# Performance work log

Hardware: AMD Instinct MI355X
Metric: run time of the kernel (lower is better)

The kernel has to match this reference:

```python
import jax, jax.numpy as jnp
import numpy as np

DN = ('NCDHW', 'OIDHW', 'NCDHW')
HEAD_COUNT = 8
LN_EPS = 1e-5


def _dwpw(x, dw_w, dw_b, pw_w, pw_b):
    # depthwise 3x3x3 conv (groups=C) followed by pointwise 1x1x1 conv, both with bias
    cin = x.shape[1]
    y = jax.lax.conv_general_dilated(x, dw_w, (1, 1, 1), [(1, 1), (1, 1), (1, 1)],
                                     dimension_numbers=DN, feature_group_count=cin)
    y = y + dw_b[None, :, None, None, None]
    y = jax.lax.conv_general_dilated(y, pw_w, (1, 1, 1), [(0, 0), (0, 0), (0, 0)],
                                     dimension_numbers=DN)
    return y + pw_b[None, :, None, None, None]


def setup_inputs() -> dict:
    key = jax.random.key(0)
    ks = iter(jax.random.split(key, 64))
    C, KC, VC = 256, 256, 256
    n, t, h, w = 4, 16, 28, 28
    d = {}
    d['input_rgb'] = jax.random.normal(next(ks), (n, C, t, h, w), dtype=jnp.float32)
    d['input_flow'] = jax.random.normal(next(ks), (n, C, t, h, w), dtype=jnp.float32)

    def conv_params(cin, cout, pfx):
        d[pfx + '_dw_w'] = jax.random.normal(next(ks), (cin, 1, 3, 3, 3), dtype=jnp.float32) * 0.05
        d[pfx + '_dw_b'] = jnp.zeros((cin,), dtype=jnp.float32)
        d[pfx + '_pw_w'] = jax.random.normal(next(ks), (cout, cin, 1, 1, 1), dtype=jnp.float32) * 0.05
        d[pfx + '_pw_b'] = jnp.zeros((cout,), dtype=jnp.float32)

    for s in ('rgb', 'flow'):
        for p, cout in (('k', KC), ('q', KC), ('v', VC)):
            conv_params(C, cout, f'{s}_{p}')
    conv_params(2 * VC, 2 * C, 'rp')
    return d


def reference(input_rgb, input_flow,
              rgb_k_dw_w, rgb_k_dw_b, rgb_k_pw_w, rgb_k_pw_b,
              rgb_q_dw_w, rgb_q_dw_b, rgb_q_pw_w, rgb_q_pw_b,
              rgb_v_dw_w, rgb_v_dw_b, rgb_v_pw_w, rgb_v_pw_b,
              flow_k_dw_w, flow_k_dw_b, flow_k_pw_w, flow_k_pw_b,
              flow_q_dw_w, flow_q_dw_b, flow_q_pw_w, flow_q_pw_b,
              flow_v_dw_w, flow_v_dw_b, flow_v_pw_w, flow_v_pw_b,
              rp_dw_w, rp_dw_b, rp_pw_w, rp_pw_b):
    n, C, t, h, w = input_rgb.shape
    S = t * h * w
    fused = jnp.concatenate([input_rgb, input_flow], axis=1)  # [n, 2C, t, h, w]

    def proj(x, dw_w, dw_b, pw_w, pw_b):
        return _dwpw(x, dw_w, dw_b, pw_w, pw_b).reshape(n, -1, S)

    keys = jnp.concatenate([proj(input_rgb, rgb_k_dw_w, rgb_k_dw_b, rgb_k_pw_w, rgb_k_pw_b),
                            proj(input_flow, flow_k_dw_w, flow_k_dw_b, flow_k_pw_w, flow_k_pw_b)], axis=1)
    queries = jnp.concatenate([proj(input_rgb, rgb_q_dw_w, rgb_q_dw_b, rgb_q_pw_w, rgb_q_pw_b),
                               proj(input_flow, flow_q_dw_w, flow_q_dw_b, flow_q_pw_w, flow_q_pw_b)], axis=1)
    values = jnp.concatenate([proj(input_rgb, rgb_v_dw_w, rgb_v_dw_b, rgb_v_pw_w, rgb_v_pw_b),
                              proj(input_flow, flow_v_dw_w, flow_v_dw_b, flow_v_pw_w, flow_v_pw_b)], axis=1)

    H = HEAD_COUNT
    hk = keys.shape[1] // H
    hv = values.shape[1] // H
    K = jax.nn.softmax(keys.reshape(n, H, hk, S), axis=3)      # softmax over sequence
    Q = jax.nn.softmax(queries.reshape(n, H, hk, S), axis=2)   # softmax over head channels
    V = values.reshape(n, H, hv, S)

    ctx = jnp.einsum('nhks,nhvs->nhkv', K, V)                   # [n,H,hk,hv]
    att = jnp.einsum('nhkv,nhks->nhvs', ctx, Q)                 # [n,H,hv,S]
    aggregated = att.reshape(n, H * hv, t, h, w)                # [n, 2*VC, t, h, w]

    rep = _dwpw(aggregated, rp_dw_w, rp_dw_b, rp_pw_w, rp_pw_b)
    x = rep + fused
    # f.layer_norm(x, x.size()): normalize over the ENTIRE tensor, no affine
    m = x.mean()
    v = x.var()
    return (x - m) / jnp.sqrt(v + LN_EPS)
```

## Files before the change

kernel.cpp:

```cpp
#include <hip/hip_runtime.h>
#include <math.h>


constexpr int NN = 4;
constexpr int C1 = 256;
constexpr int C2 = 512;
constexpr int TT = 16;
constexpr int SP = TT * 28 * 28;
constexpr long long NB = (long long)NN * C2 * SP;
constexpr int HEADS = 8;
constexpr int CTX_CHUNKS = 7;
constexpr int STATS_PARTS = 98 * 4 * 4;
constexpr double TOTAL_ELEMS = (double)NB;

typedef __attribute__((ext_vector_type(8))) short bf16x8;
typedef __attribute__((ext_vector_type(4))) short bf16x4;
typedef __attribute__((ext_vector_type(4))) float f32x4;

__device__ __forceinline__ short f2bf(float f)
{
    unsigned u = __float_as_uint(f);
    unsigned r = u + 0x7FFFu + ((u >> 16) & 1u);
    return (short)(r >> 16);
}
__device__ __forceinline__ float bf2f(short s)
{
    return __uint_as_float(((unsigned)(unsigned short)s) << 16);
}

__device__ __forceinline__ float4 loadvec4(const float* p)
{
    return *(const float4*)p;
}
__device__ __forceinline__ float4 loadvec4(const short* p)
{
    bf16x4 v = *(const bf16x4*)p;
    return (float4){bf2f(v[0]), bf2f(v[1]), bf2f(v[2]), bf2f(v[3])};
}

__device__ __forceinline__ void gload16(const short* g, short* l)
{
    __builtin_amdgcn_global_load_lds(
        (const __attribute__((address_space(1))) unsigned int*)g,
        (__attribute__((address_space(3))) unsigned int*)l,
        16, 0, 0);
}

__global__ __launch_bounds__(256)
void wcvt_kernel(const float* __restrict__ w0, const float* __restrict__ w1,
                 const float* __restrict__ w2, const float* __restrict__ w3,
                 const float* __restrict__ w4, const float* __restrict__ w5,
                 const float* __restrict__ w6, short* __restrict__ out)
{
    int i = blockIdx.x * 256 + threadIdx.x;
    if (i >= 655360) return;
    const float* src; int off;
    if (i < 393216) {
        int seg = i >> 16; off = i & 65535;
        src = seg == 0 ? w0 : seg == 1 ? w1 : seg == 2 ? w2
            : seg == 3 ? w3 : seg == 4 ? w4 : w5;
    } else { src = w6; off = i - 393216; }
    out[i] = f2bf(src[off]);
}

template<typename IT, int NSET>
__global__ __launch_bounds__(256)
void dwv_kernel(const IT* __restrict__ in,
                const float* __restrict__ w0c, const float* __restrict__ b0c,
                short* __restrict__ o0,
                const float* __restrict__ w1c, const float* __restrict__ b1c,
                short* __restrict__ o1,
                const float* __restrict__ w2c, const float* __restrict__ b2c,
                short* __restrict__ o2, int Cin)
{
    const int split = blockIdx.x, c = blockIdx.y, n = blockIdx.z;
    const int t0 = split * 8, t1 = t0 + 8;
    const int zs = (t0 - 1 > 0) ? t0 - 1 : 0;
    const int ze = (t1 < 15) ? t1 : 15;
    __shared__ float tile[2][900];
    const int tid = threadIdx.x;
    const size_t ibase = ((size_t)(n * Cin + c)) * TT * 784;
    const IT* inp = in + ibase;

    const float* wp[3] = {w0c, w1c, w2c};
    const float* bp[3] = {b0c, b1c, b2c};
    short* op[3] = {o0, o1, o2};
    float w[NSET][27], bv[NSET];
#pragma unroll
    for (int g = 0; g < NSET; ++g) {
#pragma unroll
        for (int i = 0; i < 27; ++i) w[g][i] = wp[g][c * 27 + i];
        bv[g] = bp[g][c];
    }

    for (int i = tid; i < 1800; i += 256) ((float*)tile)[i] = 0.f;

    const bool act = tid < 196;
    const int pos = tid * 4;
    const int hh = pos / 28, ww = pos - hh * 28;
    const int ladr = (hh + 1) * 30 + ww + 1;
    const int rbase = hh * 30 + ww;

    float4 preg = {0.f, 0.f, 0.f, 0.f};
    if (act) preg = loadvec4(inp + (size_t)zs * 784 + pos);

    float a0[NSET][4], a1[NSET][4], a2[NSET][4];
#pragma unroll
    for (int g = 0; g < NSET; ++g)
#pragma unroll
        for (int k = 0; k < 4; ++k) { a0[g][k] = bv[g]; a1[g][k] = bv[g]; a2[g][k] = bv[g]; }

    for (int z = zs; z <= ze; ++z) {
        float* tb = tile[z & 1];
        __syncthreads();
        if (act) {
            tb[ladr] = preg.x; tb[ladr + 1] = preg.y;
            tb[ladr + 2] = preg.z; tb[ladr + 3] = preg.w;
            if (z < ze) preg = loadvec4(inp + (size_t)(z + 1) * 784 + pos);
        }
        __syncthreads();
        if (act) {
            float v[3][6];
#pragma unroll
            for (int r = 0; r < 3; ++r)
#pragma unroll
                for (int j = 0; j < 6; ++j)
                    v[r][j] = tb[rbase + r * 30 + j];
#pragma unroll
            for (int g = 0; g < NSET; ++g)
#pragma unroll
                for (int dh = 0; dh < 3; ++dh)
#pragma unroll
                    for (int dw = 0; dw < 3; ++dw) {
                        const float wa = w[g][18 + dh * 3 + dw];
                        const float wb = w[g][9 + dh * 3 + dw];
                        const float wc2 = w[g][dh * 3 + dw];
#pragma unroll
                        for (int k = 0; k < 4; ++k) {
                            const float val = v[dh][k + dw];
                            a0[g][k] += val * wa;
                            a1[g][k] += val * wb;
                            a2[g][k] += val * wc2;
                        }
                    }
            if (z - 1 >= t0) {
#pragma unroll
                for (int g = 0; g < NSET; ++g) {
                    bf16x4 pk;
#pragma unroll
                    for (int k = 0; k < 4; ++k) pk[k] = f2bf(a0[g][k]);
                    *(bf16x4*)&op[g][ibase + (size_t)(z - 1) * 784 + pos] = pk;
                }
            }
#pragma unroll
            for (int g = 0; g < NSET; ++g)
#pragma unroll
                for (int k = 0; k < 4; ++k) {
                    a0[g][k] = a1[g][k]; a1[g][k] = a2[g][k]; a2[g][k] = bv[g];
                }
        }
    }
    if (act && ze >= t0 && ze < t1) {
#pragma unroll
        for (int g = 0; g < NSET; ++g) {
            bf16x4 pk;
#pragma unroll
            for (int k = 0; k < 4; ++k) pk[k] = f2bf(a0[g][k]);
            *(bf16x4*)&op[g][ibase + (size_t)ze * 784 + pos] = pk;
        }
    }
}

template<int MODE>
__global__ __launch_bounds__(256)
void pw_mfma_kernel(const short* __restrict__ Wb, const float* __restrict__ bias,
                    const short* __restrict__ act, short* __restrict__ outB,
                    float* __restrict__ outF, const float* __restrict__ rgb,
                    const float* __restrict__ flow, double* __restrict__ partials,
                    int Cin, size_t nStride, size_t cStride, int chOff)
{
    __shared__ short smem[34816];
    const int tid = threadIdx.x;
    const int w = tid >> 6, lane = tid & 63;
    const int s0 = blockIdx.x * 128;
    const int m0 = blockIdx.y * 128;
    const int n = blockIdx.z;
    const short* aSrc = Wb + (size_t)m0 * Cin;
    const short* bSrc = act + (size_t)n * Cin * SP;
    f32x4 acc[4][4];
#pragma unroll
    for (int i = 0; i < 4; ++i)
#pragma unroll
        for (int j = 0; j < 4; ++j)
            acc[i][j] = (f32x4){0.f, 0.f, 0.f, 0.f};
    const int lrow = lane >> 3, lslot = lane & 7;
    const int wr = w >> 1, wc = w & 1;
    const int kg = tid >> 4, scb = tid & 15;
    const int nt = Cin >> 6;

    {
        short* nA = smem;
        short* nB = smem + 16384;
#pragma unroll
        for (int cc = 0; cc < 4; ++cc) {
            const int chunk = w * 4 + cc;
            const int row = chunk * 8 + lrow;
            const int ss = lslot ^ (row & 7);
            gload16(aSrc + (size_t)row * Cin + ss * 8, &nA[chunk * 512]);
        }
        bf16x8 breg[4];
#pragma unroll
        for (int r = 0; r < 4; ++r)
            breg[r] = *(const bf16x8*)(bSrc + (size_t)(kg * 4 + r) * SP + s0 + scb * 8);
#pragma unroll
        for (int j = 0; j < 8; ++j) {
            bf16x4 pk;
#pragma unroll
            for (int r = 0; r < 4; ++r) pk[r] = breg[r][j];
            const int srow = scb * 8 + j;
            const int slot = (kg >> 1) ^ (scb & 7);
            *(bf16x4*)&nB[srow * 72 + slot * 8 + (kg & 1) * 4] = pk;
        }
    }
    __syncthreads();

    for (int t = 0; t < nt; ++t) {
        short* cA = smem + (t & 1) * 8192;
        short* cB = smem + 16384 + (t & 1) * 9216;
        short* nA = smem + ((t + 1) & 1) * 8192;
        short* nB = smem + 16384 + ((t + 1) & 1) * 9216;
        const bool more = (t + 1) < nt;
        bf16x8 bnext[4];
        if (more) {
            const int kt = (t + 1) << 6;
#pragma unroll
            for (int cc = 0; cc < 4; ++cc) {
                const int chunk = w * 4 + cc;
                const int row = chunk * 8 + lrow;
                const int ss = lslot ^ (row & 7);
                gload16(aSrc + (size_t)row * Cin + kt + ss * 8, &nA[chunk * 512]);
            }
#pragma unroll
            for (int r = 0; r < 4; ++r)
                bnext[r] = *(const bf16x8*)(bSrc + (size_t)(kt + kg * 4 + r) * SP + s0 + scb * 8);
        }
#pragma unroll
        for (int kf = 0; kf < 2; ++kf) {
            bf16x8 af[4], bfr[4];
            const int kb = kf * 4 + (lane >> 4);
#pragma unroll
            for (int i = 0; i < 4; ++i) {
                const int row = wr * 64 + i * 16 + (lane & 15);
                af[i] = *(const bf16x8*)&cA[row * 64 + ((kb ^ (row & 7)) << 3)];
            }
#pragma unroll
            for (int j = 0; j < 4; ++j) {
                const int srow = wc * 64 + j * 16 + (lane & 15);
                bfr[j] = *(const bf16x8*)&cB[srow * 72 + ((kb ^ ((srow >> 3) & 7)) << 3)];
            }
#pragma unroll
            for (int i = 0; i < 4; ++i)
#pragma unroll
                for (int j = 0; j < 4; ++j)
                    acc[i][j] = __builtin_amdgcn_mfma_f32_16x16x32_bf16(
                        af[i], bfr[j], acc[i][j], 0, 0, 0);
        }
        if (more) {
#pragma unroll
            for (int j = 0; j < 8; ++j) {
                bf16x4 pk;
#pragma unroll
                for (int r = 0; r < 4; ++r) pk[r] = bnext[r][j];
                const int srow = scb * 8 + j;
                const int slot = (kg >> 1) ^ (scb & 7);
                *(bf16x4*)&nB[srow * 72 + slot * 8 + (kg & 1) * 4] = pk;
            }
        }
        __syncthreads();
    }

    if constexpr (MODE == 0) {
        short* ep = smem;
#pragma unroll
        for (int i = 0; i < 4; ++i) {
            const int mloc = wr * 64 + i * 16 + (lane >> 4) * 4;
#pragma unroll
            for (int j = 0; j < 4; ++j) {
                const int sloc = wc * 64 + j * 16 + (lane & 15);
#pragma unroll
                for (int r = 0; r < 4; ++r)
                    ep[(mloc + r) * 136 + sloc] =
                        f2bf(acc[i][j][r] + bias[m0 + mloc + r]);
            }
        }
        __syncthreads();
        short* op = outB + (size_t)n * nStride;
#pragma unroll
        for (int cc = 0; cc < 8; ++cc) {
            const int idx = tid + cc * 256;
            const int mloc = idx >> 4, ch = idx & 15;
            bf16x8 v = *(const bf16x8*)&ep[mloc * 136 + ch * 8];
            *(bf16x8*)&op[(size_t)(chOff + m0 + mloc) * cStride + s0 + ch * 8] = v;
        }
    } else if constexpr (MODE == 1) {
        short* ep = smem;
#pragma unroll
        for (int i = 0; i < 4; ++i) {
            const int mb = wr * 64 + i * 16 + (lane >> 4) * 4;
#pragma unroll
            for (int j = 0; j < 4; ++j) {
                const int sloc = wc * 64 + j * 16 + (lane & 15);
                bf16x4 pk;
#pragma unroll
                for (int r = 0; r < 4; ++r)
                    pk[r] = f2bf(acc[i][j][r] + bias[m0 + mb + r]);
                *(bf16x4*)&ep[sloc * 136 + mb] = pk;
            }
        }
        __syncthreads();
#pragma unroll
        for (int cc = 0; cc < 8; ++cc) {
            const int idx = tid + cc * 256;
            const int sloc = idx >> 4, ch = idx & 15;
            bf16x8 v = *(const bf16x8*)&ep[sloc * 136 + ch * 8];
            *(bf16x8*)&outB[((size_t)n * SP + s0 + sloc) * 512 + chOff + m0 + ch * 8] = v;
        }
    } else {
        float* ep = (float*)smem;
        float* xp = outF + (size_t)n * C2 * SP;
        const float* rbase = (m0 < 256)
            ? rgb + ((size_t)n * 256 + m0) * SP
            : flow + ((size_t)n * 256 + (m0 - 256)) * SP;
        double ls = 0.0, lss = 0.0;
#pragma unroll
        for (int p = 0; p < 2; ++p) {
            if (p) __syncthreads();
            if (wr == p) {
#pragma unroll
                for (int i = 0; i < 4; ++i) {
                    const int mloc = i * 16 + (lane >> 4) * 4;
#pragma unroll
                    for (int j = 0; j < 4; ++j) {
                        const int sloc = wc * 64 + j * 16 + (lane & 15);
#pragma unroll
                        for (int r = 0; r < 4; ++r)
                            ep[(mloc + r) * 132 + sloc] =
                                acc[i][j][r] + bias[m0 + p * 64 + mloc + r];
                    }
                }
            }
            __syncthreads();
#pragma unroll
            for (int cc = 0; cc < 8; ++cc) {
                const int idx = tid + cc * 256;
                const int row = idx >> 5, ch = idx & 31;
                const int m = m0 + p * 64 + row;
                float4 a = *(const float4*)&ep[row * 132 + ch * 4];
                float4 rs = *(const float4*)&rbase[(size_t)(p * 64 + row) * SP + s0 + ch * 4];
                float4 x;
                x.x = a.x + rs.x; x.y = a.y + rs.y;
                x.z = a.z + rs.z; x.w = a.w + rs.w;
                *(float4*)&xp[(size_t)m * SP + s0 + ch * 4] = x;
                ls += (double)x.x + (double)x.y + (double)x.z + (double)x.w;
                lss += (double)x.x * x.x + (double)x.y * x.y +
                       (double)x.z * x.z + (double)x.w * x.w;
            }
        }
        __shared__ double s1[256], s2[256];
        s1[tid] = ls; s2[tid] = lss;
        __syncthreads();
        for (int st = 128; st > 0; st >>= 1) {
            if (tid < st) { s1[tid] += s1[tid + st]; s2[tid] += s2[tid + st]; }
            __syncthreads();
        }
        if (tid == 0) {
            const size_t bid = ((size_t)blockIdx.z * gridDim.y + blockIdx.y) *
                               gridDim.x + blockIdx.x;
            partials[2 * bid] = s1[0];
            partials[2 * bid + 1] = s2[0];
        }
    }
}

__global__ __launch_bounds__(256)
void row_stats_kernel(const short* __restrict__ K, float2* __restrict__ st)
{
    const short* p = K + (size_t)blockIdx.x * SP;
    __shared__ float sm[4];
    __shared__ float bc;
    const int tid = threadIdx.x, wv = tid >> 6, ln = tid & 63;
    float m = -1e30f;
    for (int c = tid; c < SP / 8; c += 256) {
        bf16x8 v = *(const bf16x8*)(p + c * 8);
#pragma unroll
        for (int j = 0; j < 8; ++j) m = fmaxf(m, bf2f(v[j]));
    }
    for (int o = 32; o; o >>= 1) m = fmaxf(m, __shfl_down(m, o, 64));
    if (ln == 0) sm[wv] = m;
    __syncthreads();
    if (tid == 0) bc = fmaxf(fmaxf(sm[0], sm[1]), fmaxf(sm[2], sm[3]));
    __syncthreads();
    m = bc;
    float sum = 0.f;
    for (int c = tid; c < SP / 8; c += 256) {
        bf16x8 v = *(const bf16x8*)(p + c * 8);
#pragma unroll
        for (int j = 0; j < 8; ++j) sum += __expf(bf2f(v[j]) - m);
    }
    for (int o = 32; o; o >>= 1) sum += __shfl_down(sum, o, 64);
    __syncthreads();
    if (ln == 0) sm[wv] = sum;
    __syncthreads();
    if (tid == 0) {
        float tot = sm[0] + sm[1] + sm[2] + sm[3];
        st[blockIdx.x] = (float2){m, 1.f / tot};
    }
}

__global__ __launch_bounds__(256)
void ctx_mfma_kernel(const short* __restrict__ Kb, const short* __restrict__ Vb,
                     const float2* __restrict__ stats, float* __restrict__ part)
{
    const int chunk = blockIdx.x, nh = blockIdx.y;
    const short* Kp = Kb + (size_t)nh * 64 * SP;
    const short* Vp = Vb + (size_t)nh * 64 * SP;
    __shared__ short lK[64 * 256];
    __shared__ short lV[64 * 256];
    const int tid = threadIdx.x;
    const int w = tid >> 6, lane = tid & 63;
    const int wr = w >> 1, wc = w & 1;
    f32x4 acc[2][2];
#pragma unroll
    for (int i = 0; i < 2; ++i)
#pragma unroll
        for (int j = 0; j < 2; ++j)
            acc[i][j] = (f32x4){0.f, 0.f, 0.f, 0.f};

    float km8[8], ki8[8];
#pragma unroll
    for (int ps = 0; ps < 8; ++ps) {
        float2 s = stats[nh * 64 + (tid >> 5) + ps * 8];
        km8[ps] = s.x; ki8[ps] = s.y;
    }

    for (int sub = 0; sub < 7; ++sub) {
        const int sOff = chunk * 1792 + sub * 256;
#pragma unroll
        for (int cc = 0; cc < 8; ++cc) {
            const int ch = w * 8 + cc;
            const int row = ch * 2 + (lane >> 5);
            const int sc = lane & 31;
            gload16(Vp + (size_t)row * SP + sOff + ((sc ^ (row & 7)) << 3),
                    &lV[ch * 512]);
        }
#pragma unroll
        for (int ps = 0; ps < 8; ++ps) {
            const int row = (tid >> 5) + ps * 8;
            const int sc = tid & 31;
            bf16x8 kv = *(const bf16x8*)(Kp + (size_t)row * SP + sOff + sc * 8);
            bf16x8 ev;
#pragma unroll
            for (int j = 0; j < 8; ++j)
                ev[j] = f2bf(__expf(bf2f(kv[j]) - km8[ps]) * ki8[ps]);
            *(bf16x8*)&lK[row * 256 + ((sc ^ (row & 7)) << 3)] = ev;
        }
        __syncthreads();
#pragma unroll
        for (int ks = 0; ks < 8; ++ks) {
            const int kb = ks * 4 + (lane >> 4);
            bf16x8 ak[2], bv[2];
#pragma unroll
            for (int i = 0; i < 2; ++i) {
                const int rk = wr * 32 + i * 16 + (lane & 15);
                ak[i] = *(const bf16x8*)&lK[rk * 256 + ((kb ^ (rk & 7)) << 3)];
            }
#pragma unroll
            for (int j = 0; j < 2; ++j) {
                const int rv = wc * 32 + j * 16 + (lane & 15);
                bv[j] = *(const bf16x8*)&lV[rv * 256 + ((kb ^ (rv & 7)) << 3)];
            }
#pragma unroll
            for (int i = 0; i < 2; ++i)
#pragma unroll
                for (int j = 0; j < 2; ++j)
                    acc[i][j] = __builtin_amdgcn_mfma_f32_16x16x32_bf16(
                        ak[i], bv[j], acc[i][j], 0, 0, 0);
        }
        __syncthreads();
    }
    float* op = part + ((size_t)nh * CTX_CHUNKS + chunk) * 4096;
#pragma unroll
    for (int i = 0; i < 2; ++i)
#pragma unroll
        for (int j = 0; j < 2; ++j)
#pragma unroll
            for (int r = 0; r < 4; ++r) {
                const int k = wr * 32 + i * 16 + (lane >> 4) * 4 + r;
                const int v = wc * 32 + j * 16 + (lane & 15);
                op[k * 64 + v] = acc[i][j][r];
            }
}

__global__ __launch_bounds__(256)
void ctx_reduce_kernel(const float* __restrict__ part, float* __restrict__ ctx)
{
    const int nh = blockIdx.x;
    for (int e = threadIdx.x; e < 4096; e += 256) {
        float s = 0.f;
        for (int c = 0; c < CTX_CHUNKS; ++c)
            s += part[((size_t)nh * CTX_CHUNKS + c) * 4096 + e];
        ctx[(size_t)nh * 4096 + e] = s;
    }
}

__global__ __launch_bounds__(256)
void att_kernel(const float* __restrict__ ctx, const short* __restrict__ Qb,
                short* __restrict__ out)
{
    const int nh = blockIdx.y;
    const int n = nh >> 3, h = nh & 7;
    const int s0 = blockIdx.x * 64;
    const float* cp = ctx + (size_t)nh * 4096;
    __shared__ short lC[64 * 64];
    __shared__ short lQ[64 * 64];
    __shared__ float red[64][4];
    __shared__ short lO[64 * 72];
    const int tid = threadIdx.x;
    const int w = tid >> 6, lane = tid & 63;

#pragma unroll
    for (int u = 0; u < 2; ++u) {
        const int si = (tid >> 6) + u * 4;
        const int v = tid & 63;
        bf16x8 pk;
#pragma unroll
        for (int j = 0; j < 8; ++j) pk[j] = f2bf(cp[(si * 8 + j) * 64 + v]);
        *(bf16x8*)&lC[v * 64 + ((si ^ (v & 7)) << 3)] = pk;
    }
    const int sq = tid >> 2, qpart = tid & 3;
    const short* Qrow = Qb + ((size_t)n * SP + s0 + sq) * 512 + h * 64 + qpart * 16;
    bf16x8 q0 = *(const bf16x8*)(Qrow);
    bf16x8 q1 = *(const bf16x8*)(Qrow + 8);
    float e[16];
    float mx = -1e30f;
#pragma unroll
    for (int j = 0; j < 8; ++j) {
        e[j] = bf2f(q0[j]); e[8 + j] = bf2f(q1[j]);
        mx = fmaxf(mx, fmaxf(e[j], e[8 + j]));
    }
    red[sq][qpart] = mx;
    __syncthreads();
    mx = fmaxf(fmaxf(red[sq][0], red[sq][1]), fmaxf(red[sq][2], red[sq][3]));
    float sum = 0.f;
#pragma unroll
    for (int j = 0; j < 16; ++j) { e[j] = __expf(e[j] - mx); sum += e[j]; }
    __syncthreads();
    red[sq][qpart] = sum;
    __syncthreads();
    const float sinv = 1.f / (red[sq][0] + red[sq][1] + red[sq][2] + red[sq][3]);
    bf16x8 p0, p1;
#pragma unroll
    for (int j = 0; j < 8; ++j) {
        p0[j] = f2bf(e[j] * sinv);
        p1[j] = f2bf(e[8 + j] * sinv);
    }
    *(bf16x8*)&lQ[sq * 64 + (((qpart * 2) ^ (sq & 7)) << 3)] = p0;
    *(bf16x8*)&lQ[sq * 64 + (((qpart * 2 + 1) ^ (sq & 7)) << 3)] = p1;
    __syncthreads();

    f32x4 acc[4];
#pragma unroll
    for (int i = 0; i < 4; ++i) acc[i] = (f32x4){0.f, 0.f, 0.f, 0.f};
    const int srow = w * 16 + (lane & 15);
#pragma unroll
    for (int ks = 0; ks < 2; ++ks) {
        const int kb = ks * 4 + (lane >> 4);
        bf16x8 bq = *(const bf16x8*)&lQ[srow * 64 + ((kb ^ (srow & 7)) << 3)];
#pragma unroll
        for (int i = 0; i < 4; ++i) {
            const int vr = i * 16 + (lane & 15);
            bf16x8 av = *(const bf16x8*)&lC[vr * 64 + ((kb ^ (vr & 7)) << 3)];
            acc[i] = __builtin_amdgcn_mfma_f32_16x16x32_bf16(av, bq, acc[i], 0, 0, 0);
        }
    }
#pragma unroll
    for (int i = 0; i < 4; ++i)
#pragma unroll
        for (int r = 0; r < 4; ++r)
            lO[(i * 16 + (lane >> 4) * 4 + r) * 72 + w * 16 + (lane & 15)] =
                f2bf(acc[i][r]);
    __syncthreads();
    short* op = out + (size_t)nh * 64 * SP;
#pragma unroll
    for (int cc = 0; cc < 2; ++cc) {
        const int idx = tid + cc * 256;
        const int v = idx >> 3, ch = idx & 7;
        bf16x8 t = *(const bf16x8*)&lO[v * 72 + ch * 8];
        *(bf16x8*)&op[(size_t)v * SP + s0 + ch * 8] = t;
    }
}

__global__ __launch_bounds__(256)
void stats_final_kernel(const double* __restrict__ partials, float* __restrict__ mv)
{
    double ls = 0.0, lss = 0.0;
    for (int i = threadIdx.x; i < STATS_PARTS; i += 256) {
        ls += partials[2 * i];
        lss += partials[2 * i + 1];
    }
    __shared__ double s1[256], s2[256];
    const int tid = threadIdx.x;
    s1[tid] = ls; s2[tid] = lss;
    __syncthreads();
    for (int s = 128; s > 0; s >>= 1) {
        if (tid < s) { s1[tid] += s1[tid + s]; s2[tid] += s2[tid + s]; }
        __syncthreads();
    }
    if (tid == 0) {
        double mean = s1[0] / TOTAL_ELEMS;
        double var = s2[0] / TOTAL_ELEMS - mean * mean;
        mv[0] = (float)mean;
        mv[1] = (float)(1.0 / sqrt(var + 1e-5));
    }
}

__global__ __launch_bounds__(256)
void normalize_kernel(float* __restrict__ x, const float* __restrict__ mv)
{
    const float mean = mv[0], inv = mv[1];
    size_t i = ((size_t)blockIdx.x * 256 + threadIdx.x) * 4;
    const size_t tot = (size_t)NB;
    const size_t step = (size_t)gridDim.x * 1024;
    for (; i < tot; i += step) {
        float4 v = *(float4*)&x[i];
        v.x = (v.x - mean) * inv; v.y = (v.y - mean) * inv;
        v.z = (v.z - mean) * inv; v.w = (v.w - mean) * inv;
        *(float4*)&x[i] = v;
    }
}

extern "C" void kernel_launch(void* const* d_in, const int* in_sizes, int n_in,
                              void* d_out, int out_size, void* d_ws, size_t ws_size,
                              hipStream_t stream)
{
    (void)in_sizes; (void)n_in; (void)out_size; (void)ws_size;
    const float* rgb = (const float*)d_in[0];
    const float* flow = (const float*)d_in[1];
    float* ws = (float*)d_ws;

    short* bufK = (short*)ws;
    short* bufQ = (short*)(ws + NB / 2);
    short* bufV = (short*)(ws + NB);
    short* actK = (short*)(ws + 3 * NB / 2);
    short* actQ = (short*)(ws + 7 * NB / 4);
    short* actV = (short*)(ws + 2 * NB);
    short* wB   = (short*)(ws + 9 * NB / 4);
    float2* rowStats = (float2*)(wB + 655360);
    float* ctxBuf = (float*)(rowStats + 2048);
    double* partials = (double*)(ctxBuf + 32 * 4096);
    float* mv = (float*)(partials + 2 * STATS_PARTS);
    float* ctxPart = ws + 3 * NB / 2;
    short* rpDw = actK;

    const size_t nsA = (size_t)C2 * SP, csA = SP;

    wcvt_kernel<<<2560, 256, 0, stream>>>(
        (const float*)d_in[4], (const float*)d_in[12], (const float*)d_in[16],
        (const float*)d_in[24], (const float*)d_in[8], (const float*)d_in[20],
        (const float*)d_in[28], wB);

    for (int st = 0; st < 2; ++st) {
        const float* src = st ? flow : rgb;
        const int kI = st ? 14 : 2, qI = st ? 18 : 6, vI = st ? 22 : 10;
        const int choff = st ? 256 : 0;
        dwv_kernel<float, 3><<<dim3(2, C1, NN), 256, 0, stream>>>(
            src,
            (const float*)d_in[kI], (const float*)d_in[kI + 1], actK,
            (const float*)d_in[qI], (const float*)d_in[qI + 1], actQ,
            (const float*)d_in[vI], (const float*)d_in[vI + 1], actV, C1);
        pw_mfma_kernel<0><<<dim3(SP / 128, 2, NN), 256, 0, stream>>>(
            wB + (size_t)(st ? 2 : 0) * 65536, (const float*)d_in[kI + 3], actK,
            bufK, nullptr, nullptr, nullptr, nullptr, C1, nsA, csA, choff);
        pw_mfma_kernel<0><<<dim3(SP / 128, 2, NN), 256, 0, stream>>>(
            wB + (size_t)(st ? 3 : 1) * 65536, (const float*)d_in[vI + 3], actV,
            bufV, nullptr, nullptr, nullptr, nullptr, C1, nsA, csA, choff);
        pw_mfma_kernel<1><<<dim3(SP / 128, 2, NN), 256, 0, stream>>>(
            wB + (size_t)(st ? 5 : 4) * 65536, (const float*)d_in[qI + 3], actQ,
            bufQ, nullptr, nullptr, nullptr, nullptr, C1, 0, 0, choff);
    }

    row_stats_kernel<<<NN * C2, 256, 0, stream>>>(bufK, rowStats);
    ctx_mfma_kernel<<<dim3(CTX_CHUNKS, NN * HEADS), 256, 0, stream>>>(
        bufK, bufV, rowStats, ctxPart);
    ctx_reduce_kernel<<<NN * HEADS, 256, 0, stream>>>(ctxPart, ctxBuf);
    att_kernel<<<dim3(SP / 64, NN * HEADS), 256, 0, stream>>>(
        ctxBuf, bufQ, bufV);

    dwv_kernel<short, 1><<<dim3(2, C2, NN), 256, 0, stream>>>(
        bufV, (const float*)d_in[26], (const float*)d_in[27], rpDw,
        nullptr, nullptr, nullptr, nullptr, nullptr, nullptr, C2);
    pw_mfma_kernel<2><<<dim3(SP / 128, 4, NN), 256, 0, stream>>>(
        wB + 6 * 65536, (const float*)d_in[29], rpDw, nullptr,
        (float*)d_out, rgb, flow, partials, C2, 0, 0, 0);

    stats_final_kernel<<<1, 256, 0, stream>>>(partials, mv);
    normalize_kernel<<<2048, 256, 0, stream>>>((float*)d_out, mv);
}
```

Measured before the change: 443.7 us.

## Fuse K softmax stats into K/V pointwise GEMM, bf16 intermediate before normalize

Merges the K and V pointwise GEMMs into a single launch and computes per-block online-softmax partial max/sum for K in the epilogue. A small reduce kernel then replaces the full re-read of K done by row_stats_kernel. The final pointwise epilogue now writes the residual sum as bf16 to a workspace buffer instead of fp32 to the output, and uses a remapped 1D grid to improve locality. The normalize pass reads bf16 and writes fp32, cutting memory traffic, at the cost of rounding the pre-normalization values to bf16.

Result: faster. 419.3 us (median of 2 runs) (-5.5%).

```diff
diff --git a/kernel.cpp b/kernel.cpp
--- a/kernel.cpp
+++ b/kernel.cpp
@@ -10,7 +10,8 @@
 constexpr long long NB = (long long)NN * C2 * SP;
 constexpr int HEADS = 8;
 constexpr int CTX_CHUNKS = 7;
-constexpr int STATS_PARTS = 98 * 4 * 4;
+constexpr int SBLKS = 98;
+constexpr int STATS_PARTS = SBLKS * 4 * 4;
 constexpr double TOTAL_ELEMS = (double)NB;
 
 typedef __attribute__((ext_vector_type(8))) short bf16x8;
@@ -173,20 +174,37 @@
 
 template<int MODE>
 __global__ __launch_bounds__(256)
-void pw_mfma_kernel(const short* __restrict__ Wb, const float* __restrict__ bias,
-                    const short* __restrict__ act, short* __restrict__ outB,
-                    float* __restrict__ outF, const float* __restrict__ rgb,
-                    const float* __restrict__ flow, double* __restrict__ partials,
+void pw_mfma_kernel(const short* __restrict__ WbA, const float* __restrict__ biasA,
+                    const short* __restrict__ actA, short* __restrict__ outA,
+                    const short* __restrict__ WbV, const float* __restrict__ biasV,
+                    const short* __restrict__ actV, short* __restrict__ outV,
+                    const float* __restrict__ rgb, const float* __restrict__ flow,
+                    double* __restrict__ partials, float2* __restrict__ kpart,
                     int Cin, size_t nStride, size_t cStride, int chOff)
 {
     __shared__ short smem[34816];
     const int tid = threadIdx.x;
     const int w = tid >> 6, lane = tid & 63;
-    const int s0 = blockIdx.x * 128;
-    const int m0 = blockIdx.y * 128;
-    const int n = blockIdx.z;
+    int s0, m0, n, seg = 0, sBlk;
+    if constexpr (MODE == 2) {
+        const int b = blockIdx.x;
+        const int r = b & 7, t = b >> 3;
+        const int mBlk = t & 3, q = t >> 2;
+        const int g = q * 8 + r;
+        n = g / SBLKS; sBlk = g % SBLKS;
+        s0 = sBlk * 128; m0 = mBlk * 128;
+    } else {
+        sBlk = blockIdx.x; s0 = sBlk * 128; n = blockIdx.z;
+        if constexpr (MODE == 0) { seg = blockIdx.y >> 1; m0 = (blockIdx.y & 1) * 128; }
+        else m0 = blockIdx.y * 128;
+    }
+    const short* Wb = (MODE == 0 && seg) ? WbV : WbA;
+    const float* bias = (MODE == 0 && seg) ? biasV : biasA;
+    const short* actp = (MODE == 0 && seg) ? actV : actA;
+    short* outB = (MODE == 0 && seg) ? outV : outA;
+
     const short* aSrc = Wb + (size_t)m0 * Cin;
-    const short* bSrc = act + (size_t)n * Cin * SP;
+    const short* bSrc = actp + (size_t)n * Cin * SP;
     f32x4 acc[4][4];
 #pragma unroll
     for (int i = 0; i < 4; ++i)
@@ -302,6 +320,23 @@
             bf16x8 v = *(const bf16x8*)&ep[mloc * 136 + ch * 8];
             *(bf16x8*)&op[(size_t)(chOff + m0 + mloc) * cStride + s0 + ch * 8] = v;
         }
+        if (seg == 0) {
+            const int row = tid >> 1, half = tid & 1;
+            const short* rp = &ep[row * 136 + half * 64];
+            float mx = -1e30f;
+#pragma unroll 8
+            for (int j = 0; j < 64; ++j) mx = fmaxf(mx, bf2f(rp[j]));
+            float sum = 0.f;
+#pragma unroll 8
+            for (int j = 0; j < 64; ++j) sum += __expf(bf2f(rp[j]) - mx);
+            const float mo = __shfl_xor(mx, 1, 64);
+            const float so = __shfl_xor(sum, 1, 64);
+            const float mg = fmaxf(mx, mo);
+            const float sg = sum * __expf(mx - mg) + so * __expf(mo - mg);
+            if (half == 0)
+                kpart[(size_t)(n * 512 + chOff + m0 + row) * SBLKS + sBlk] =
+                    (float2){mg, sg};
+        }
     } else if constexpr (MODE == 1) {
         short* ep = smem;
 #pragma unroll
@@ -323,47 +358,46 @@
             const int idx = tid + cc * 256;
             const int sloc = idx >> 4, ch = idx & 15;
             bf16x8 v = *(const bf16x8*)&ep[sloc * 136 + ch * 8];
-            *(bf16x8*)&outB[((size_t)n * SP + s0 + sloc) * 512 + chOff + m0 + ch * 8] = v;
+            *(bf16x8*)&outA[((size_t)n * SP + s0 + sloc) * 512 + chOff + m0 + ch * 8] = v;
         }
     } else {
         float* ep = (float*)smem;
-        float* xp = outF + (size_t)n * C2 * SP;
+#pragma unroll
+        for (int i = 0; i < 4; ++i) {
+            const int mloc = wr * 64 + i * 16 + (lane >> 4) * 4;
+#pragma unroll
+            for (int j = 0; j < 4; ++j) {
+                const int sloc = wc * 64 + j * 16 + (lane & 15);
+#pragma unroll
+                for (int r = 0; r < 4; ++r)
+                    ep[(mloc + r) * 132 + sloc] =
+                        acc[i][j][r] + bias[m0 + mloc + r];
+            }
+        }
+        __syncthreads();
+        short* xo = outA + (size_t)n * C2 * SP;
         const float* rbase = (m0 < 256)
             ? rgb + ((size_t)n * 256 + m0) * SP
             : flow + ((size_t)n * 256 + (m0 - 256)) * SP;
         double ls = 0.0, lss = 0.0;
 #pragma unroll
-        for (int p = 0; p < 2; ++p) {
-            if (p) __syncthreads();
-            if (wr == p) {
-#pragma unroll
-                for (int i = 0; i < 4; ++i) {
-                    const int mloc = i * 16 + (lane >> 4) * 4;
-#pragma unroll
-                    for (int j = 0; j < 4; ++j) {
-                        const int sloc = wc * 64 + j * 16 + (lane & 15);
-#pragma unroll
-                        for (int r = 0; r < 4; ++r)
-                            ep[(mloc + r) * 132 + sloc] =
-                                acc[i][j][r] + bias[m0 + p * 64 + mloc + r];
-                    }
-                }
-            }
-            __syncthreads();
-#pragma unroll
-            for (int cc = 0; cc < 8; ++cc) {
-                const int idx = tid + cc * 256;
-                const int row = idx >> 5, ch = idx & 31;
-                const int m = m0 + p * 64 + row;
-                float4 a = *(const float4*)&ep[row * 132 + ch * 4];
-                float4 rs = *(const float4*)&rbase[(size_t)(p * 64 + row) * SP + s0 + ch * 4];
-                float4 x;
-                x.x = a.x + rs.x; x.y = a.y + rs.y;
-                x.z = a.z + rs.z; x.w = a.w + rs.w;
-                *(float4*)&xp[(size_t)m * SP + s0 + ch * 4] = x;
-                ls += (double)x.x + (double)x.y + (double)x.z + (double)x.w;
-                lss += (double)x.x * x.x + (double)x.y * x.y +
-                       (double)x.z * x.z + (double)x.w * x.w;
+        for (int cc = 0; cc < 8; ++cc) {
+            const int idx = tid + cc * 256;
+            const int mloc = idx >> 4, ch = idx & 15;
+            float4 a0 = *(const float4*)&ep[mloc * 132 + ch * 8];
+            float4 a1 = *(const float4*)&ep[mloc * 132 + ch * 8 + 4];
+            float4 r0 = *(const float4*)&rbase[(size_t)mloc * SP + s0 + ch * 8];
+            float4 r1 = *(const float4*)&rbase[(size_t)mloc * SP + s0 + ch * 8 + 4];
+            bf16x8 pk;
+            pk[0] = f2bf(a0.x + r0.x); pk[1] = f2bf(a0.y + r0.y);
+            pk[2] = f2bf(a0.z + r0.z); pk[3] = f2bf(a0.w + r0.w);
+            pk[4] = f2bf(a1.x + r1.x); pk[5] = f2bf(a1.y + r1.y);
+            pk[6] = f2bf(a1.z + r1.z); pk[7] = f2bf(a1.w + r1.w);
+            *(bf16x8*)&xo[(size_t)(m0 + mloc) * SP + s0 + ch * 8] = pk;
+#pragma unroll
+            for (int k = 0; k < 8; ++k) {
+                const double xv = (double)bf2f(pk[k]);
+                ls += xv; lss += xv * xv;
             }
         }
         __shared__ double s1[256], s2[256];
@@ -374,47 +408,25 @@
             __syncthreads();
         }
         if (tid == 0) {
-            const size_t bid = ((size_t)blockIdx.z * gridDim.y + blockIdx.y) *
-                               gridDim.x + blockIdx.x;
-            partials[2 * bid] = s1[0];
-            partials[2 * bid + 1] = s2[0];
-        }
-    }
-}
-
-__global__ __launch_bounds__(256)
-void row_stats_kernel(const short* __restrict__ K, float2* __restrict__ st)
-{
-    const short* p = K + (size_t)blockIdx.x * SP;
-    __shared__ float sm[4];
-    __shared__ float bc;
-    const int tid = threadIdx.x, wv = tid >> 6, ln = tid & 63;
-    float m = -1e30f;
-    for (int c = tid; c < SP / 8; c += 256) {
-        bf16x8 v = *(const bf16x8*)(p + c * 8);
-#pragma unroll
-        for (int j = 0; j < 8; ++j) m = fmaxf(m, bf2f(v[j]));
-    }
-    for (int o = 32; o; o >>= 1) m = fmaxf(m, __shfl_down(m, o, 64));
-    if (ln == 0) sm[wv] = m;
-    __syncthreads();
-    if (tid == 0) bc = fmaxf(fmaxf(sm[0], sm[1]), fmaxf(sm[2], sm[3]));
-    __syncthreads();
-    m = bc;
-    float sum = 0.f;
-    for (int c = tid; c < SP / 8; c += 256) {
-        bf16x8 v = *(const bf16x8*)(p + c * 8);
-#pragma unroll
-        for (int j = 0; j < 8; ++j) sum += __expf(bf2f(v[j]) - m);
-    }
-    for (int o = 32; o; o >>= 1) sum += __shfl_down(sum, o, 64);
-    __syncthreads();
-    if (ln == 0) sm[wv] = sum;
-    __syncthreads();
-    if (tid == 0) {
-        float tot = sm[0] + sm[1] + sm[2] + sm[3];
-        st[blockIdx.x] = (float2){m, 1.f / tot};
-    }
+            partials[2 * blockIdx.x] = s1[0];
+            partials[2 * blockIdx.x + 1] = s2[0];
+        }
+    }
+}
+
+__global__ __launch_bounds__(256)
+void kstats_reduce_kernel(const float2* __restrict__ kpart, float2* __restrict__ st)
+{
+    const int row = blockIdx.x * 256 + threadIdx.x;
+    const float2* p = kpart + (size_t)row * SBLKS;
+    float m = -1e30f, s = 0.f;
+    for (int b = 0; b < SBLKS; ++b) {
+        float2 e = p[b];
+        float nm = fmaxf(m, e.x);
+        s = s * __expf(m - nm) + e.y * __expf(e.x - nm);
+        m = nm;
+    }
+    st[row] = (float2){m, 1.f / s};
 }
 
 __global__ __launch_bounds__(256)
@@ -625,17 +637,22 @@
 }
 
 __global__ __launch_bounds__(256)
-void normalize_kernel(float* __restrict__ x, const float* __restrict__ mv)
+void normalize_kernel(const short* __restrict__ xb, float* __restrict__ out,
+                      const float* __restrict__ mv)
 {
     const float mean = mv[0], inv = mv[1];
-    size_t i = ((size_t)blockIdx.x * 256 + threadIdx.x) * 4;
+    size_t i = ((size_t)blockIdx.x * 256 + threadIdx.x) * 8;
     const size_t tot = (size_t)NB;
-    const size_t step = (size_t)gridDim.x * 1024;
+    const size_t step = (size_t)gridDim.x * 2048;
     for (; i < tot; i += step) {
-        float4 v = *(float4*)&x[i];
-        v.x = (v.x - mean) * inv; v.y = (v.y - mean) * inv;
-        v.z = (v.z - mean) * inv; v.w = (v.w - mean) * inv;
-        *(float4*)&x[i] = v;
+        bf16x8 v = *(const bf16x8*)&xb[i];
+        float4 a, b;
+        a.x = (bf2f(v[0]) - mean) * inv; a.y = (bf2f(v[1]) - mean) * inv;
+        a.z = (bf2f(v[2]) - mean) * inv; a.w = (bf2f(v[3]) - mean) * inv;
+        b.x = (bf2f(v[4]) - mean) * inv; b.y = (bf2f(v[5]) - mean) * inv;
+        b.z = (bf2f(v[6]) - mean) * inv; b.w = (bf2f(v[7]) - mean) * inv;
+        *(float4*)&out[i] = a;
+        *(float4*)&out[i + 4] = b;
     }
 }
 
@@ -659,8 +676,10 @@
     float* ctxBuf = (float*)(rowStats + 2048);
     double* partials = (double*)(ctxBuf + 32 * 4096);
     float* mv = (float*)(partials + 2 * STATS_PARTS);
+    float2* kpart = (float2*)(mv + 8);
     float* ctxPart = ws + 3 * NB / 2;
     short* rpDw = actK;
+    short* xb = bufK;
 
     const size_t nsA = (size_t)C2 * SP, csA = SP;
 
@@ -678,18 +697,17 @@
             (const float*)d_in[kI], (const float*)d_in[kI + 1], actK,
             (const float*)d_in[qI], (const float*)d_in[qI + 1], actQ,
             (const float*)d_in[vI], (const float*)d_in[vI + 1], actV, C1);
-        pw_mfma_kernel<0><<<dim3(SP / 128, 2, NN), 256, 0, stream>>>(
-            wB + (size_t)(st ? 2 : 0) * 65536, (const float*)d_in[kI + 3], actK,
-            bufK, nullptr, nullptr, nullptr, nullptr, C1, nsA, csA, choff);
-        pw_mfma_kernel<0><<<dim3(SP / 128, 2, NN), 256, 0, stream>>>(
-            wB + (size_t)(st ? 3 : 1) * 65536, (const float*)d_in[vI + 3], actV,
-            bufV, nullptr, nullptr, nullptr, nullptr, C1, nsA, csA, choff);
-        pw_mfma_kernel<1><<<dim3(SP / 128, 2, NN), 256, 0, stream>>>(
-            wB + (size_t)(st ? 5 : 4) * 65536, (const float*)d_in[qI + 3], actQ,
-            bufQ, nullptr, nullptr, nullptr, nullptr, C1, 0, 0, choff);
-    }
-
-    row_stats_kernel<<<NN * C2, 256, 0, stream>>>(bufK, rowStats);
+        pw_mfma_kernel<0><<<dim3(SBLKS, 4, NN), 256, 0, stream>>>(
+            wB + (size_t)(st ? 2 : 0) * 65536, (const float*)d_in[kI + 3], actK, bufK,
+            wB + (size_t)(st ? 3 : 1) * 65536, (const float*)d_in[vI + 3], actV, bufV,
+            nullptr, nullptr, nullptr, kpart, C1, nsA, csA, choff);
+        pw_mfma_kernel<1><<<dim3(SBLKS, 2, NN), 256, 0, stream>>>(
+            wB + (size_t)(st ? 5 : 4) * 65536, (const float*)d_in[qI + 3], actQ, bufQ,
+            nullptr, nullptr, nullptr, nullptr,
+            nullptr, nullptr, nullptr, nullptr, C1, 0, 0, choff);
+    }
+
+    kstats_reduce_kernel<<<8, 256, 0, stream>>>(kpart, rowStats);
     ctx_mfma_kernel<<<dim3(CTX_CHUNKS, NN * HEADS), 256, 0, stream>>>(
         bufK, bufV, rowStats, ctxPart);
     ctx_reduce_kernel<<<NN * HEADS, 256, 0, stream>>>(ctxPart, ctxBuf);
@@ -699,10 +717,11 @@
     dwv_kernel<short, 1><<<dim3(2, C2, NN), 256, 0, stream>>>(
         bufV, (const float*)d_in[26], (const float*)d_in[27], rpDw,
         nullptr, nullptr, nullptr, nullptr, nullptr, nullptr, C2);
-    pw_mfma_kernel<2><<<dim3(SP / 128, 4, NN), 256, 0, stream>>>(
-        wB + 6 * 65536, (const float*)d_in[29], rpDw, nullptr,
-        (float*)d_out, rgb, flow, partials, C2, 0, 0, 0);
+    pw_mfma_kernel<2><<<STATS_PARTS, 256, 0, stream>>>(
+        wB + 6 * 65536, (const float*)d_in[29], rpDw, xb,
+        nullptr, nullptr, nullptr, nullptr,
+        rgb, flow, partials, nullptr, C2, 0, 0, 0);
 
     stats_final_kernel<<<1, 256, 0, stream>>>(partials, mv);
-    normalize_kernel<<<2048, 256, 0, stream>>>((float*)d_out, mv);
-}
+    normalize_kernel<<<2048, 256, 0, stream>>>(xb, (float*)d_out, mv);
+}
```
